# Optimization experiments

Measured on AMD Instinct MI355X. Metric: run time of the kernel, lower is better.

## Reference

```python
import jax, jax.numpy as jnp
import numpy as np

BS = 2048; N = 16; IN = 128; H = 128; M = 64; A = 32; IMSG = 64; NNH = 256; NA = 30; CB = 64

def _lin(x, w, b):
    return x @ w.T + b

def _bn(x, g, b):
    # BatchNorm1d in training mode: batch statistics, biased variance, eps=1e-5
    m = x.mean(0)
    v = x.var(0)
    return (x - m) / jnp.sqrt(v + 1e-5) * g + b

_lrelu = jax.nn.leaky_relu  # default negative_slope=0.01 matches torch LeakyReLU


def setup_inputs() -> dict:
    key = jax.random.key(0)
    ks = iter(jax.random.split(key, 32))
    def w(shape):
        return jax.random.normal(next(ks), shape, jnp.float32) / np.sqrt(shape[-1]).astype(np.float32)
    R = BS * N
    return {
        'inputs': jax.random.normal(next(ks), (R, IN), jnp.float32),
        'hidden_state': jax.random.normal(next(ks), (R, H), jnp.float32),
        'latent_state': jax.random.normal(next(ks), (R, CB), jnp.float32),
        'eps': jax.random.normal(next(ks), (R, M), jnp.float32),
        'fc1_w': w((H, IN)), 'fc1_b': jnp.zeros((H,), jnp.float32),
        'w_ih': w((3 * H, H)), 'w_hh': w((3 * H, H)),
        'b_ih': jnp.zeros((3 * H,), jnp.float32), 'b_hh': jnp.zeros((3 * H,), jnp.float32),
        'lse_w1': w((H, CB)), 'lse_b1': jnp.zeros((H,), jnp.float32),
        'lse_w2': w((H, H)), 'lse_b2': jnp.zeros((H,), jnp.float32),
        'me_w1': w((NNH, 2 * H)), 'me_b1': jnp.zeros((NNH,), jnp.float32),
        'me_g': jnp.ones((NNH,), jnp.float32), 'me_beta': jnp.zeros((NNH,), jnp.float32),
        'me_w2': w((2 * M, NNH)), 'me_b2': jnp.zeros((2 * M,), jnp.float32),
        'k_w': w((A, H)), 'k_b': jnp.zeros((A,), jnp.float32),
        'q_w': w((A, M)), 'q_b': jnp.zeros((A,), jnp.float32),
        'v_w1': w((NNH, H + M)), 'v_b1': jnp.zeros((NNH,), jnp.float32),
        'v_w2': w((IMSG, NNH)), 'v_b2': jnp.zeros((IMSG,), jnp.float32),
        'fc2_w': w((NA, 2 * H + IMSG * N)), 'fc2_b': jnp.zeros((NA,), jnp.float32),
        'n_agents': N,
    }


def reference(inputs, hidden_state, latent_state, eps,
              fc1_w, fc1_b, w_ih, w_hh, b_ih, b_hh,
              lse_w1, lse_b1, lse_w2, lse_b2,
              me_w1, me_b1, me_g, me_beta, me_w2, me_b2,
              k_w, k_b, q_w, q_b, v_w1, v_b1, v_w2, v_b2,
              fc2_w, fc2_b, n_agents):
    n = n_agents
    R = inputs.shape[0]
    bs = R // n
    # calc_hidden: fc1 + relu, then GRUCell
    x = jax.nn.relu(_lin(inputs, fc1_w, fc1_b))
    gi = _lin(x, w_ih, b_ih)
    gh = _lin(hidden_state, w_hh, b_hh)
    ir, iz, inn = jnp.split(gi, 3, axis=-1)
    hr, hz, hn = jnp.split(gh, 3, axis=-1)
    r = jax.nn.sigmoid(ir + hr)
    z = jax.nn.sigmoid(iz + hz)
    ng = jnp.tanh(inn + r * hn)
    h = ng + z * (hidden_state - ng)  # [R, H]
    # latent_state_encoder
    latent_emb = _lin(jax.nn.relu(_lin(latent_state, lse_w1, lse_b1)), lse_w2, lse_b2)
    le_d = jax.lax.stop_gradient(latent_emb)  # .detach() in source
    # msg_encoder -> clamped Normal params -> rsample
    t = _lrelu(_bn(_lin(jnp.concatenate([h, le_d], -1), me_w1, me_b1), me_g, me_beta))
    t = _lrelu(_lin(t, me_w2, me_b2))
    Md = eps.shape[-1]
    mean = jnp.clip(t[:, :Md], -1.0, 1.0)
    std = jnp.clip(t[:, Md:], 0.5, 1.0)
    pm = mean + std * eps  # personal_msg per agent, [R, M]
    # attn_message_integration: value/query at pair (i,j) depend only on sender j,
    # so compute once per sender and broadcast (same math as repeat in source).
    value = _lin(_lrelu(_lin(jnp.concatenate([h, pm], -1), v_w1, v_b1)), v_w2, v_b2).reshape(bs, n, -1)
    keyv = _lin(h, k_w, k_b).reshape(bs, n, -1)
    qv = _lin(pm, q_w, q_b).reshape(bs, n, -1)
    kh = keyv / jnp.maximum(jnp.linalg.norm(keyv, axis=-1, keepdims=True), 1e-8)
    qh = qv / jnp.maximum(jnp.linalg.norm(qv, axis=-1, keepdims=True), 1e-8)
    alpha = jax.nn.softmax(jnp.einsum('bia,bja->bij', kh, qh), axis=-1)  # cosine attn
    diag_mask = 1.0 - jnp.eye(n, dtype=alpha.dtype)  # zero self-messages
    msg = (alpha * diag_mask)[..., None] * value[:, None, :, :]  # [bs, n, n, IMSG]
    msg = msg.reshape(R, -1)
    return _lin(jnp.concatenate([h, latent_emb, msg], -1), fc2_w, fc2_b)  # q: [R, NA]
```

## Files before the change

kernel.cpp:

```cpp
#include <hip/hip_runtime.h>
#include <math.h>

namespace {
constexpr int R_ = 32768;
constexpr int N_ = 16;
constexpr int NA_ = 30;
constexpr int BSB_ = R_ / N_;
constexpr int NB64_ = R_ / 64;
}

typedef __bf16 bf16x8 __attribute__((ext_vector_type(8)));
typedef float f32x4 __attribute__((ext_vector_type(4)));

__device__ inline unsigned int f2bf(float f) {
    unsigned int u = __float_as_uint(f);
    return (u + 0x7fffu + ((u >> 16) & 1u)) >> 16;
}
__device__ inline float bf2f(unsigned int us) {
    return __uint_as_float(us << 16);
}
__device__ inline unsigned int pack2(float a, float b) {
    return f2bf(a) | (f2bf(b) << 16);
}
__device__ inline uint4 pack8(float4 f0, float4 f1) {
    uint4 u;
    u.x = pack2(f0.x, f0.y); u.y = pack2(f0.z, f0.w);
    u.z = pack2(f1.x, f1.y); u.w = pack2(f1.z, f1.w);
    return u;
}
__device__ inline float fsig(float x)  { return __builtin_amdgcn_rcpf(1.f + __expf(-x)); }
__device__ inline float ftanh(float x) { return 1.f - 2.f * __builtin_amdgcn_rcpf(__expf(2.f * x) + 1.f); }

__device__ __forceinline__ bf16x8 lda_frag(const uint4* At, int KC, int row, int c) {
    return __builtin_bit_cast(bf16x8, At[(row * KC + c) ^ (row & 7)]);
}
__device__ __forceinline__ bf16x8 ldb_frag(const unsigned short* W, int row, int rstride, int c) {
    return __builtin_bit_cast(bf16x8, *(const uint4*)(W + (size_t)row * rstride + (size_t)c * 8));
}

namespace woff {
constexpr unsigned fc1 = 0;
constexpr unsigned ih  = 16384;
constexpr unsigned hh  = 65536;
constexpr unsigned l1  = 114688;
constexpr unsigned l2  = 122880;
constexpr unsigned m1  = 139264;
constexpr unsigned m2  = 204800;
constexpr unsigned kw  = 237568;
constexpr unsigned qw  = 241664;
constexpr unsigned v1  = 243712;
constexpr unsigned v2  = 292864;
constexpr unsigned f2  = 309248;
constexpr unsigned total = 347648;
}

__global__ __launch_bounds__(256)
void wcvt_kernel(const float* __restrict__ fc1_w, const float* __restrict__ w_ih,
                 const float* __restrict__ w_hh, const float* __restrict__ lse_w1,
                 const float* __restrict__ lse_w2, const float* __restrict__ me_w1,
                 const float* __restrict__ me_w2, const float* __restrict__ k_w,
                 const float* __restrict__ q_w, const float* __restrict__ v_w1,
                 const float* __restrict__ v_w2, const float* __restrict__ fc2_w,
                 unsigned short* __restrict__ dst)
{
    unsigned i = blockIdx.x * 256 + threadIdx.x;
    if (i >= woff::total) return;
    const float* src; unsigned base;
    if      (i < woff::ih) { src = fc1_w;  base = woff::fc1; }
    else if (i < woff::hh) { src = w_ih;   base = woff::ih; }
    else if (i < woff::l1) { src = w_hh;   base = woff::hh; }
    else if (i < woff::l2) { src = lse_w1; base = woff::l1; }
    else if (i < woff::m1) { src = lse_w2; base = woff::l2; }
    else if (i < woff::m2) { src = me_w1;  base = woff::m1; }
    else if (i < woff::kw) { src = me_w2;  base = woff::m2; }
    else if (i < woff::qw) { src = k_w;    base = woff::kw; }
    else if (i < woff::v1) { src = q_w;    base = woff::qw; }
    else if (i < woff::v2) { src = v_w1;   base = woff::v1; }
    else if (i < woff::f2) { src = v_w2;   base = woff::v2; }
    else                   { src = fc2_w;  base = woff::f2; }
    dst[i] = (unsigned short)f2bf(src[i - base]);
}

__global__ __launch_bounds__(512, 4)
void stage1(const float* __restrict__ inputs, const float* __restrict__ hidden,
            const unsigned short* __restrict__ fc1w, const float* __restrict__ fc1_b,
            const unsigned short* __restrict__ wih, const unsigned short* __restrict__ whh,
            const float* __restrict__ b_ih, const float* __restrict__ b_hh,
            unsigned short* __restrict__ hb,
            const float* __restrict__ latent,
            const unsigned short* __restrict__ w1b, const float* __restrict__ b1,
            const unsigned short* __restrict__ w2b, const float* __restrict__ b2,
            unsigned short* __restrict__ leb)
{
    __shared__ uint4 shbuf[64 * 48];
    const int tid = threadIdx.x;
    const int lane = tid & 63, w = tid >> 6;
    const int m = lane & 15, g = lane >> 4;

    if (blockIdx.x < (unsigned)NB64_) {
        uint4* Ain   = shbuf;
        uint4* Atile = shbuf + 64 * 16;
        const int r0 = blockIdx.x * 64;

        for (int idx = tid; idx < 64 * 16; idx += 512) {
            int row = idx >> 4, c = idx & 15;
            const float4* p = (const float4*)(inputs + (size_t)(r0 + row) * 128 + c * 8);
            Ain[(row * 16 + c) ^ (row & 7)] = pack8(p[0], p[1]);
            const float4* ph = (const float4*)(hidden + (size_t)(r0 + row) * 128 + c * 8);
            Atile[(row * 32 + (16 + c)) ^ (row & 7)] = pack8(ph[0], ph[1]);
        }
        __syncthreads();

        {
            f32x4 acc[4] = {};
            #pragma unroll
            for (int ks = 0; ks < 4; ++ks) {
                bf16x8 bf = ldb_frag(fc1w, w * 16 + m, 128, ks * 4 + g);
                #pragma unroll
                for (int fr = 0; fr < 4; ++fr) {
                    bf16x8 af = lda_frag(Ain, 16, fr * 16 + m, ks * 4 + g);
                    acc[fr] = __builtin_amdgcn_mfma_f32_16x16x32_bf16(af, bf, acc[fr], 0, 0, 0);
                }
            }
            int col = w * 16 + m;
            float bv = fc1_b[col];
            int c = col >> 3, el = col & 7;
            #pragma unroll
            for (int fr = 0; fr < 4; ++fr) {
                #pragma unroll
                for (int i = 0; i < 4; ++i) {
                    int row = fr * 16 + g * 4 + i;
                    float v = acc[fr][i] + bv;
                    v = v > 0.f ? v : 0.f;
                    ((unsigned short*)Atile)[((row * 32 + c) ^ (row & 7)) * 8 + el] =
                        (unsigned short)f2bf(v);
                }
            }
        }
        __syncthreads();

        {
            f32x4 rr[4] = {}, zz[4] = {}, ni[4] = {}, nh[4] = {};
            const int ro = w * 16 + m;
            #pragma unroll
            for (int ks = 0; ks < 4; ++ks) {
                bf16x8 brr = ldb_frag(wih, ro, 128, ks * 4 + g);
                bf16x8 bzz = ldb_frag(wih, 128 + ro, 128, ks * 4 + g);
                bf16x8 bnn = ldb_frag(wih, 256 + ro, 128, ks * 4 + g);
                #pragma unroll
                for (int fr = 0; fr < 4; ++fr) {
                    bf16x8 af = lda_frag(Atile, 32, fr * 16 + m, ks * 4 + g);
                    rr[fr] = __builtin_amdgcn_mfma_f32_16x16x32_bf16(af, brr, rr[fr], 0, 0, 0);
                    zz[fr] = __builtin_amdgcn_mfma_f32_16x16x32_bf16(af, bzz, zz[fr], 0, 0, 0);
                    ni[fr] = __builtin_amdgcn_mfma_f32_16x16x32_bf16(af, bnn, ni[fr], 0, 0, 0);
                }
            }
            #pragma unroll
            for (int ks = 0; ks < 4; ++ks) {
                bf16x8 brr = ldb_frag(whh, ro, 128, ks * 4 + g);
                bf16x8 bzz = ldb_frag(whh, 128 + ro, 128, ks * 4 + g);
                bf16x8 bnn = ldb_frag(whh, 256 + ro, 128, ks * 4 + g);
                #pragma unroll
                for (int fr = 0; fr < 4; ++fr) {
                    bf16x8 af = lda_frag(Atile, 32, fr * 16 + m, 16 + ks * 4 + g);
                    rr[fr] = __builtin_amdgcn_mfma_f32_16x16x32_bf16(af, brr, rr[fr], 0, 0, 0);
                    zz[fr] = __builtin_amdgcn_mfma_f32_16x16x32_bf16(af, bzz, zz[fr], 0, 0, 0);
                    nh[fr] = __builtin_amdgcn_mfma_f32_16x16x32_bf16(af, bnn, nh[fr], 0, 0, 0);
                }
            }
            {
                int c = ro;
                float brz = b_ih[c] + b_hh[c];
                float bzz2 = b_ih[128 + c] + b_hh[128 + c];
                float bin = b_ih[256 + c], bhn = b_hh[256 + c];
                int hc = 16 + (c >> 3), hel = c & 7;
                #pragma unroll
                for (int fr = 0; fr < 4; ++fr) {
                    #pragma unroll
                    for (int i = 0; i < 4; ++i) {
                        int row = fr * 16 + g * 4 + i;
                        float rv = fsig(rr[fr][i] + brz);
                        float zv = fsig(zz[fr][i] + bzz2);
                        float ng = ftanh(ni[fr][i] + bin + rv * (nh[fr][i] + bhn));
                        float hp = bf2f(((unsigned short*)Atile)[((row * 32 + hc) ^ (row & 7)) * 8 + hel]);
                        float hv = ng + zv * (hp - ng);
                        hb[(size_t)(r0 + row) * 128 + c] = (unsigned short)f2bf(hv);
                    }
                }
            }
        }
    } else {
        uint4* Alat = shbuf;
        uint4* Alt  = shbuf + 64 * 8;
        const int r0 = (blockIdx.x - NB64_) * 64;

        {
            int row = tid >> 3, c = tid & 7;
            const float4* p = (const float4*)(latent + (size_t)(r0 + row) * 64 + c * 8);
            Alat[(row * 8 + c) ^ (row & 7)] = pack8(p[0], p[1]);
        }
        __syncthreads();

        {
            f32x4 acc[4] = {};
            #pragma unroll
            for (int ks = 0; ks < 2; ++ks) {
                bf16x8 bf = ldb_frag(w1b, w * 16 + m, 64, ks * 4 + g);
                #pragma unroll
                for (int fr = 0; fr < 4; ++fr) {
                    bf16x8 af = lda_frag(Alat, 8, fr * 16 + m, ks * 4 + g);
                    acc[fr] = __builtin_amdgcn_mfma_f32_16x16x32_bf16(af, bf, acc[fr], 0, 0, 0);
                }
            }
            int col = w * 16 + m;
            float bv = b1[col];
            int c = col >> 3, el = col & 7;
            #pragma unroll
            for (int fr = 0; fr < 4; ++fr) {
                #pragma unroll
                for (int i = 0; i < 4; ++i) {
                    int row = fr * 16 + g * 4 + i;
                    float v = acc[fr][i] + bv;
                    v = v > 0.f ? v : 0.f;
                    ((unsigned short*)Alt)[((row * 16 + c) ^ (row & 7)) * 8 + el] =
                        (unsigned short)f2bf(v);
                }
            }
        }
        __syncthreads();

        {
            f32x4 acc[4] = {};
            #pragma unroll
            for (int ks = 0; ks < 4; ++ks) {
                bf16x8 bf = ldb_frag(w2b, w * 16 + m, 128, ks * 4 + g);
                #pragma unroll
                for (int fr = 0; fr < 4; ++fr) {
                    bf16x8 af = lda_frag(Alt, 16, fr * 16 + m, ks * 4 + g);
                    acc[fr] = __builtin_amdgcn_mfma_f32_16x16x32_bf16(af, bf, acc[fr], 0, 0, 0);
                }
            }
            int col = w * 16 + m;
            float bv = b2[col];
            #pragma unroll
            for (int fr = 0; fr < 4; ++fr) {
                #pragma unroll
                for (int i = 0; i < 4; ++i) {
                    int rowl = fr * 16 + g * 4 + i;
                    float v = acc[fr][i] + bv;
                    leb[(size_t)(r0 + rowl) * 128 + col] = (unsigned short)f2bf(v);
                }
            }
        }
    }
}

__global__ __launch_bounds__(512, 4)
void me1_stats(const unsigned short* __restrict__ hb, const unsigned short* __restrict__ leb,
               const unsigned short* __restrict__ W, const float* __restrict__ bias,
               const unsigned short* __restrict__ f2w, const float* __restrict__ fc2_b,
               unsigned short* __restrict__ t1,
               float* __restrict__ psum, float* __restrict__ psq,
               float* __restrict__ hl)
{
    __shared__ uint4 Atile[64 * 32];
    __shared__ uint4 T1b[64 * 32];
    const int tid = threadIdx.x;
    const int r0 = blockIdx.x * 64;

    for (int idx = tid; idx < 64 * 16; idx += 512) {
        int row = idx >> 4, c = idx & 15;
        Atile[(row * 32 + c) ^ (row & 7)] =
            *(const uint4*)(hb + (size_t)(r0 + row) * 128 + c * 8);
        Atile[(row * 32 + (16 + c)) ^ (row & 7)] =
            *(const uint4*)(leb + (size_t)(r0 + row) * 128 + c * 8);
    }
    __syncthreads();

    const int lane = tid & 63, w = tid >> 6;
    const int m = lane & 15, g = lane >> 4;
    unsigned short* t1s = (unsigned short*)T1b;

    {
        const int o0 = w * 32;
        f32x4 acc[4][2] = {};
        #pragma unroll
        for (int ks = 0; ks < 8; ++ks) {
            bf16x8 bf[2];
            #pragma unroll
            for (int fc = 0; fc < 2; ++fc)
                bf[fc] = ldb_frag(W, o0 + fc * 16 + m, 256, ks * 4 + g);
            #pragma unroll
            for (int fr = 0; fr < 4; ++fr) {
                bf16x8 af = lda_frag(Atile, 32, fr * 16 + m, ks * 4 + g);
                #pragma unroll
                for (int fc = 0; fc < 2; ++fc)
                    acc[fr][fc] = __builtin_amdgcn_mfma_f32_16x16x32_bf16(
                        af, bf[fc], acc[fr][fc], 0, 0, 0);
            }
        }
        #pragma unroll
        for (int fc = 0; fc < 2; ++fc) {
            int col = o0 + fc * 16 + m;
            float bv = bias[col];
            float s = 0.f, q = 0.f;
            #pragma unroll
            for (int fr = 0; fr < 4; ++fr) {
                #pragma unroll
                for (int i = 0; i < 4; ++i) {
                    int rowl = fr * 16 + g * 4 + i;
                    float v = acc[fr][fc][i] + bv;
                    t1s[rowl * 256 + col] = (unsigned short)f2bf(v);
                    s += v; q += v * v;
                }
            }
            s += __shfl_xor(s, 16); s += __shfl_xor(s, 32);
            q += __shfl_xor(q, 16); q += __shfl_xor(q, 32);
            if (lane < 16) {
                psum[(size_t)blockIdx.x * 256 + col] = s;
                psq[(size_t)blockIdx.x * 256 + col] = q;
            }
        }
    }
    __syncthreads();
    for (int idx = tid; idx < 64 * 32; idx += 512) {
        int row = idx >> 5, c = idx & 31;
        *(uint4*)(t1 + (size_t)(r0 + row) * 256 + c * 8) = T1b[row * 32 + c];
    }

    if (w < 4) {
        f32x4 acc[2] = {};
        #pragma unroll
        for (int ks = 0; ks < 8; ++ks) {
            bf16x8 af = lda_frag(Atile, 32, w * 16 + m, ks * 4 + g);
            bf16x8 bf[2];
            #pragma unroll
            for (int fc = 0; fc < 2; ++fc) {
                int col = fc * 16 + m;
                bf[fc] = (col < NA_) ? ldb_frag(f2w, col, 1280, ks * 4 + g) : bf16x8{};
            }
            #pragma unroll
            for (int fc = 0; fc < 2; ++fc)
                acc[fc] = __builtin_amdgcn_mfma_f32_16x16x32_bf16(af, bf[fc], acc[fc], 0, 0, 0);
        }
        #pragma unroll
        for (int fc = 0; fc < 2; ++fc) {
            int col = fc * 16 + m;
            if (col < NA_) {
                float bv = fc2_b[col];
                #pragma unroll
                for (int i = 0; i < 4; ++i) {
                    int row = r0 + w * 16 + g * 4 + i;
                    hl[(size_t)row * NA_ + col] = acc[fc][i] + bv;
                }
            }
        }
    }
}

__global__ __launch_bounds__(256)
void bn_final_kernel(const float* __restrict__ psum, const float* __restrict__ psq,
                     const float* __restrict__ g, const float* __restrict__ beta,
                     float* __restrict__ scale, float* __restrict__ shift)
{
    __shared__ float redS[4], redQ[4];
    const int f = blockIdx.x;
    const int tid = threadIdx.x;
    float s = 0.f, q = 0.f;
    for (int b = tid; b < NB64_; b += 256) {
        s += psum[(size_t)b * 256 + f];
        q += psq[(size_t)b * 256 + f];
    }
    #pragma unroll
    for (int off = 32; off >= 1; off >>= 1) {
        s += __shfl_down(s, off);
        q += __shfl_down(q, off);
    }
    if ((tid & 63) == 0) { redS[tid >> 6] = s; redQ[tid >> 6] = q; }
    __syncthreads();
    if (tid == 0) {
        s = redS[0] + redS[1] + redS[2] + redS[3];
        q = redQ[0] + redQ[1] + redQ[2] + redQ[3];
        float mean = s / (float)R_;
        float var = q / (float)R_ - mean * mean;
        float istd = rsqrtf(var + 1e-5f);
        float sc = g[f] * istd;
        scale[f] = sc;
        shift[f] = beta[f] - mean * sc;
    }
}

__global__ __launch_bounds__(512, 4)
void me2kqv(const unsigned short* __restrict__ t1,
            const float* __restrict__ scale, const float* __restrict__ shift,
            const unsigned short* __restrict__ W2, const float* __restrict__ me2_b,
            const float* __restrict__ eps,
            const unsigned short* __restrict__ hb,
            const unsigned short* __restrict__ kwb, const float* __restrict__ k_b,
            const unsigned short* __restrict__ qwb, const float* __restrict__ q_b,
            const unsigned short* __restrict__ v1w, const float* __restrict__ v1_b,
            const unsigned short* __restrict__ v2w, const float* __restrict__ v2_b,
            float* __restrict__ kh, float* __restrict__ qh,
            unsigned short* __restrict__ valb)
{
    __shared__ uint4 bufA[64 * 32];
    __shared__ uint4 bufB[64 * 24];
    __shared__ float sc_s[256], sh_s[256];
    const int tid = threadIdx.x;
    const int r0 = blockIdx.x * 64;
    const int lane = tid & 63, w = tid >> 6;
    const int m = lane & 15, g = lane >> 4;

    if (tid < 256) { sc_s[tid] = scale[tid]; sh_s[tid] = shift[tid]; }
    for (int idx = tid; idx < 64 * 16; idx += 512) {
        int row = idx >> 4, c = idx & 15;
        bufB[(row * 24 + c) ^ (row & 7)] =
            *(const uint4*)(hb + (size_t)(r0 + row) * 128 + c * 8);
    }
    __syncthreads();

    for (int idx = tid; idx < 64 * 32; idx += 512) {
        int row = idx >> 5, c = idx & 31;
        uint4 u = *(const uint4*)(t1 + (size_t)(r0 + row) * 256 + c * 8);
        unsigned int vv[4] = {u.x, u.y, u.z, u.w};
        float f[8];
        #pragma unroll
        for (int q2 = 0; q2 < 4; ++q2) {
            f[2 * q2]     = __uint_as_float((vv[q2] & 0xffffu) << 16);
            f[2 * q2 + 1] = __uint_as_float(vv[q2] & 0xffff0000u);
        }
        int k = c * 8;
        #pragma unroll
        for (int j = 0; j < 8; ++j) {
            float v = f[j] * sc_s[k + j] + sh_s[k + j];
            f[j] = v > 0.f ? v : 0.01f * v;
        }
        uint4 r;
        r.x = pack2(f[0], f[1]); r.y = pack2(f[2], f[3]);
        r.z = pack2(f[4], f[5]); r.w = pack2(f[6], f[7]);
        bufA[(row * 32 + c) ^ (row & 7)] = r;
    }
    __syncthreads();

    {
        const int colm = w * 16 + m;
        f32x4 acc[4] = {};
        #pragma unroll
        for (int ks = 0; ks < 8; ++ks) {
            bf16x8 bf = ldb_frag(W2, colm, 256, ks * 4 + g);
            #pragma unroll
            for (int fr = 0; fr < 4; ++fr) {
                bf16x8 af = lda_frag(bufA, 32, fr * 16 + m, ks * 4 + g);
                acc[fr] = __builtin_amdgcn_mfma_f32_16x16x32_bf16(af, bf, acc[fr], 0, 0, 0);
            }
        }
        float bv = me2_b[colm];
        __syncthreads();
        float* meanS = (float*)bufA;
        if (w < 4) {
            #pragma unroll
            for (int fr = 0; fr < 4; ++fr) {
                #pragma unroll
                for (int i = 0; i < 4; ++i) {
                    int row = fr * 16 + g * 4 + i;
                    float vm = acc[fr][i] + bv;
                    vm = vm > 0.f ? vm : 0.01f * vm;
                    vm = fminf(fmaxf(vm, -1.f), 1.f);
                    meanS[row * 64 + colm] = vm;
                }
            }
        }
        __syncthreads();
        if (w >= 4) {
            int cp = colm - 64;
            int hc = 16 + (cp >> 3), hel = cp & 7;
            #pragma unroll
            for (int fr = 0; fr < 4; ++fr) {
                #pragma unroll
                for (int i = 0; i < 4; ++i) {
                    int row = fr * 16 + g * 4 + i;
                    float vs = acc[fr][i] + bv;
                    vs = vs > 0.f ? vs : 0.01f * vs;
                    vs = fminf(fmaxf(vs, 0.5f), 1.f);
                    float e = eps[(size_t)(r0 + row) * 64 + cp];
                    float vm = meanS[row * 64 + cp];
                    ((unsigned short*)bufB)[((row * 24 + hc) ^ (row & 7)) * 8 + hel] =
                        (unsigned short)f2bf(vm + vs * e);
                }
            }
        }
    }
    __syncthreads();

    if (w < 4) {
        const bool isq = (w >= 2);
        const int rbase = (w & 1) * 32;
        f32x4 acc[2][2] = {};
        const int nks = isq ? 2 : 4;
        for (int ks = 0; ks < nks; ++ks) {
            bf16x8 af[2], bf[2];
            #pragma unroll
            for (int fr = 0; fr < 2; ++fr)
                af[fr] = lda_frag(bufB, 24, rbase + fr * 16 + m, (isq ? 16 : 0) + ks * 4 + g);
            #pragma unroll
            for (int fc = 0; fc < 2; ++fc)
                bf[fc] = isq ? ldb_frag(qwb, fc * 16 + m, 64, ks * 4 + g)
                             : ldb_frag(kwb, fc * 16 + m, 128, ks * 4 + g);
            #pragma unroll
            for (int fr = 0; fr < 2; ++fr)
                #pragma unroll
                for (int fc = 0; fc < 2; ++fc)
                    acc[fr][fc] = __builtin_amdgcn_mfma_f32_16x16x32_bf16(
                        af[fr], bf[fc], acc[fr][fc], 0, 0, 0);
        }
        const float* bias = isq ? q_b : k_b;
        float b0 = bias[m], b1 = bias[16 + m];
        float* outp = isq ? qh : kh;
        #pragma unroll
        for (int fr = 0; fr < 2; ++fr) {
            #pragma unroll
            for (int i = 0; i < 4; ++i) {
                float v0 = acc[fr][0][i] + b0;
                float v1 = acc[fr][1][i] + b1;
                float ss = v0 * v0 + v1 * v1;
                ss += __shfl_xor(ss, 1); ss += __shfl_xor(ss, 2);
                ss += __shfl_xor(ss, 4); ss += __shfl_xor(ss, 8);
                float inv = 1.f / fmaxf(sqrtf(ss), 1e-8f);
                int row = r0 + rbase + fr * 16 + g * 4 + i;
                outp[(size_t)row * 32 + m] = v0 * inv;
                outp[(size_t)row * 32 + 16 + m] = v1 * inv;
            }
        }
    }

    {
        const int o0 = w * 32;
        f32x4 acc[4][2] = {};
        #pragma unroll
        for (int ks = 0; ks < 6; ++ks) {
            bf16x8 bf[2];
            #pragma unroll
            for (int fc = 0; fc < 2; ++fc)
                bf[fc] = ldb_frag(v1w, o0 + fc * 16 + m, 192, ks * 4 + g);
            #pragma unroll
            for (int fr = 0; fr < 4; ++fr) {
                bf16x8 af = lda_frag(bufB, 24, fr * 16 + m, ks * 4 + g);
                #pragma unroll
                for (int fc = 0; fc < 2; ++fc)
                    acc[fr][fc] = __builtin_amdgcn_mfma_f32_16x16x32_bf16(
                        af, bf[fc], acc[fr][fc], 0, 0, 0);
            }
        }
        #pragma unroll
        for (int fc = 0; fc < 2; ++fc) {
            int col = o0 + fc * 16 + m;
            float bv = v1_b[col];
            int c = col >> 3, el = col & 7;
            #pragma unroll
            for (int fr = 0; fr < 4; ++fr) {
                #pragma unroll
                for (int i = 0; i < 4; ++i) {
                    int row = fr * 16 + g * 4 + i;
                    float v = acc[fr][fc][i] + bv;
                    v = v > 0.f ? v : 0.01f * v;
                    ((unsigned short*)bufA)[((row * 32 + c) ^ (row & 7)) * 8 + el] =
                        (unsigned short)f2bf(v);
                }
            }
        }
    }
    __syncthreads();

    {
        const int col = (w & 3) * 16 + m;
        const int rbase = (w >> 2) * 32;
        f32x4 acc[2] = {};
        #pragma unroll
        for (int ks = 0; ks < 8; ++ks) {
            bf16x8 bf = ldb_frag(v2w, col, 256, ks * 4 + g);
            #pragma unroll
            for (int fr = 0; fr < 2; ++fr) {
                bf16x8 af = lda_frag(bufA, 32, rbase + fr * 16 + m, ks * 4 + g);
                acc[fr] = __builtin_amdgcn_mfma_f32_16x16x32_bf16(af, bf, acc[fr], 0, 0, 0);
            }
        }
        float bv = v2_b[col];
        unsigned short* vb = (unsigned short*)bufB;
        #pragma unroll
        for (int fr = 0; fr < 2; ++fr) {
            #pragma unroll
            for (int i = 0; i < 4; ++i) {
                int rowl = rbase + fr * 16 + g * 4 + i;
                vb[rowl * 64 + col] = (unsigned short)f2bf(acc[fr][i] + bv);
            }
        }
    }
    __syncthreads();
    {
        int row = tid >> 3, c = tid & 7;
        *(uint4*)(valb + (size_t)(r0 + row) * 64 + c * 8) = ((uint4*)bufB)[row * 8 + c];
    }
}

__global__ __launch_bounds__(256)
void vproj_kernel(const unsigned short* __restrict__ value, const float* __restrict__ w2,
                  float* __restrict__ vproj)
{
    __shared__ float w2s[NA_][65];
    __shared__ float val_s[64][65];
    const int tid = threadIdx.x;
    const int j = blockIdx.x & 15;
    const int b0 = (blockIdx.x >> 4) * 64;

    for (int idx = tid; idx < NA_ * 64; idx += 256) {
        int na = idx >> 6, k = idx & 63;
        w2s[na][k] = w2[(size_t)na * 1280 + 256 + j * 64 + k];
    }
    for (int idx = tid; idx < 64 * 64; idx += 256) {
        int bl = idx >> 6, k = idx & 63;
        val_s[bl][k] = bf2f(value[((size_t)(b0 + bl) * 16 + j) * 64 + k]);
    }
    __syncthreads();

    for (int task = tid; task < 64 * NA_; task += 256) {
        int bl = task / NA_, na = task - bl * NA_;
        float acc = 0.f;
        #pragma unroll 16
        for (int k = 0; k < 64; ++k) acc = fmaf(val_s[bl][k], w2s[na][k], acc);
        vproj[((size_t)(b0 + bl) * 16 + j) * NA_ + na] = acc;
    }
}

__global__ __launch_bounds__(256)
void attn_combine(const float* __restrict__ kh, const float* __restrict__ qh,
                  const float* __restrict__ vproj, const float* __restrict__ hl,
                  float* __restrict__ outv)
{
    __shared__ float kh_s[16][33], qh_s[16][33];
    __shared__ float al_s[16][16];
    __shared__ float vp_s[16][NA_];
    const int tid = threadIdx.x;
    const size_t rb = (size_t)blockIdx.x * 16;

    for (int idx = tid; idx < 512; idx += 256) {
        int r = idx >> 5, a = idx & 31;
        kh_s[r][a] = kh[rb * 32 + idx];
        qh_s[r][a] = qh[rb * 32 + idx];
    }
    for (int idx = tid; idx < 16 * NA_; idx += 256)
        vp_s[idx / NA_][idx % NA_] = vproj[rb * NA_ + idx];
    __syncthreads();

    {
        int i = tid >> 4, j = tid & 15;
        float l = 0.f;
        #pragma unroll
        for (int a = 0; a < 32; ++a) l = fmaf(kh_s[i][a], qh_s[j][a], l);
        float mx = l;
        #pragma unroll
        for (int mm = 8; mm >= 1; mm >>= 1) mx = fmaxf(mx, __shfl_xor(mx, mm));
        float e = __expf(l - mx);
        float s = e;
        #pragma unroll
        for (int mm = 8; mm >= 1; mm >>= 1) s += __shfl_xor(s, mm);
        float a = e / s;
        if (i == j) a = 0.f;
        al_s[i][j] = a;
    }
    __syncthreads();

    for (int task = tid; task < 16 * NA_; task += 256) {
        int i = task / NA_, na = task - i * NA_;
        float acc = hl[(rb + i) * NA_ + na];
        #pragma unroll
        for (int j = 0; j < 16; ++j) acc = fmaf(al_s[i][j], vp_s[j][na], acc);
        outv[(rb + i) * NA_ + na] = acc;
    }
}

extern "C" void kernel_launch(void* const* d_in, const int* in_sizes, int n_in,
                              void* d_out, int out_size, void* d_ws, size_t ws_size,
                              hipStream_t stream)
{
    (void)in_sizes; (void)n_in; (void)out_size; (void)ws_size;
    const float* inputs  = (const float*)d_in[0];
    const float* hidden  = (const float*)d_in[1];
    const float* latent  = (const float*)d_in[2];
    const float* eps     = (const float*)d_in[3];
    const float* fc1_w   = (const float*)d_in[4];
    const float* fc1_b   = (const float*)d_in[5];
    const float* w_ih    = (const float*)d_in[6];
    const float* w_hh    = (const float*)d_in[7];
    const float* b_ih    = (const float*)d_in[8];
    const float* b_hh    = (const float*)d_in[9];
    const float* lse_w1  = (const float*)d_in[10];
    const float* lse_b1  = (const float*)d_in[11];
    const float* lse_w2  = (const float*)d_in[12];
    const float* lse_b2  = (const float*)d_in[13];
    const float* me_w1   = (const float*)d_in[14];
    const float* me_b1   = (const float*)d_in[15];
    const float* me_g    = (const float*)d_in[16];
    const float* me_beta = (const float*)d_in[17];
    const float* me_w2   = (const float*)d_in[18];
    const float* me_b2   = (const float*)d_in[19];
    const float* k_w     = (const float*)d_in[20];
    const float* k_b     = (const float*)d_in[21];
    const float* q_w     = (const float*)d_in[22];
    const float* q_b     = (const float*)d_in[23];
    const float* v_w1    = (const float*)d_in[24];
    const float* v_b1    = (const float*)d_in[25];
    const float* v_w2    = (const float*)d_in[26];
    const float* v_b2    = (const float*)d_in[27];
    const float* fc2_w   = (const float*)d_in[28];
    const float* fc2_b   = (const float*)d_in[29];

    const size_t R = R_;
    unsigned short* bws = (unsigned short*)d_ws;
    unsigned short* hb   = bws;
    unsigned short* leb  = hb + R * 128;
    unsigned short* t1b  = leb + R * 128;
    unsigned short* valb = t1b + R * 256;
    unsigned short* wb   = valb + R * 64;
    float* fws  = (float*)(wb + woff::total);
    float* khf  = fws;
    float* qhf  = khf + R * 32;
    float* hlf  = qhf + R * 32;
    float* vpf  = hlf + R * 30;
    float* psum = vpf + R * 30;
    float* psq  = psum + (size_t)NB64_ * 256;
    float* scale = psq + (size_t)NB64_ * 256;
    float* shift = scale + 256;

    dim3 blk(256);
    dim3 g512(NB64_);

    wcvt_kernel<<<dim3((woff::total + 255) / 256), blk, 0, stream>>>(
        fc1_w, w_ih, w_hh, lse_w1, lse_w2, me_w1, me_w2, k_w, q_w, v_w1, v_w2, fc2_w, wb);

    stage1<<<dim3(2 * NB64_), dim3(512), 0, stream>>>(
        inputs, hidden, wb + woff::fc1, fc1_b, wb + woff::ih, wb + woff::hh,
        b_ih, b_hh, hb,
        latent, wb + woff::l1, lse_b1, wb + woff::l2, lse_b2, leb);
    me1_stats<<<g512, dim3(512), 0, stream>>>(hb, leb, wb + woff::m1, me_b1,
                                              wb + woff::f2, fc2_b, t1b, psum, psq, hlf);
    bn_final_kernel<<<dim3(256), blk, 0, stream>>>(psum, psq, me_g, me_beta, scale, shift);
    me2kqv<<<g512, dim3(512), 0, stream>>>(t1b, scale, shift, wb + woff::m2, me_b2, eps,
                                           hb, wb + woff::kw, k_b, wb + woff::qw, q_b,
                                           wb + woff::v1, v_b1, wb + woff::v2, v_b2,
                                           khf, qhf, valb);
    vproj_kernel<<<dim3(16 * (BSB_ / 64)), blk, 0, stream>>>(valb, fc2_w, vpf);
    attn_combine<<<dim3(BSB_), blk, 0, stream>>>(khf, qhf, vpf, hlf, (float*)d_out);
}
```

Before: 110.0 us.

## Fuse value projection and attention combine into me2 kernel tail

Folds vproj_kernel and attn_combine into the end of the me2kqv kernel, now called me2tail. Each 64-row block holds four complete 16-agent groups, so kh/qh stay in shared memory and the value-times-fc2 projection and softmax attention run locally. This removes two launches and the global round-trips of kh, qh, value and vproj. In exchange it adds shared memory (khs/qhs arrays), which may lower occupancy. The vproj step now reads fc2 weights as fp32 straight from global per thread instead of staging them in shared memory.

```diff
diff --git a/kernel.cpp b/kernel.cpp
--- a/kernel.cpp
+++ b/kernel.cpp
@@ -391,20 +391,21 @@
 }
 
 __global__ __launch_bounds__(512, 4)
-void me2kqv(const unsigned short* __restrict__ t1,
-            const float* __restrict__ scale, const float* __restrict__ shift,
-            const unsigned short* __restrict__ W2, const float* __restrict__ me2_b,
-            const float* __restrict__ eps,
-            const unsigned short* __restrict__ hb,
-            const unsigned short* __restrict__ kwb, const float* __restrict__ k_b,
-            const unsigned short* __restrict__ qwb, const float* __restrict__ q_b,
-            const unsigned short* __restrict__ v1w, const float* __restrict__ v1_b,
-            const unsigned short* __restrict__ v2w, const float* __restrict__ v2_b,
-            float* __restrict__ kh, float* __restrict__ qh,
-            unsigned short* __restrict__ valb)
+void me2tail(const unsigned short* __restrict__ t1,
+             const float* __restrict__ scale, const float* __restrict__ shift,
+             const unsigned short* __restrict__ W2, const float* __restrict__ me2_b,
+             const float* __restrict__ eps,
+             const unsigned short* __restrict__ hb,
+             const unsigned short* __restrict__ kwb, const float* __restrict__ k_b,
+             const unsigned short* __restrict__ qwb, const float* __restrict__ q_b,
+             const unsigned short* __restrict__ v1w, const float* __restrict__ v1_b,
+             const unsigned short* __restrict__ v2w, const float* __restrict__ v2_b,
+             const float* __restrict__ w2f, const float* __restrict__ hl,
+             float* __restrict__ outv)
 {
     __shared__ uint4 bufA[64 * 32];
     __shared__ uint4 bufB[64 * 24];
+    __shared__ float khs[64][33], qhs[64][33];
     __shared__ float sc_s[256], sh_s[256];
     const int tid = threadIdx.x;
     const int r0 = blockIdx.x * 64;
@@ -515,7 +516,6 @@
         }
         const float* bias = isq ? q_b : k_b;
         float b0 = bias[m], b1 = bias[16 + m];
-        float* outp = isq ? qh : kh;
         #pragma unroll
         for (int fr = 0; fr < 2; ++fr) {
             #pragma unroll
@@ -526,9 +526,9 @@
                 ss += __shfl_xor(ss, 1); ss += __shfl_xor(ss, 2);
                 ss += __shfl_xor(ss, 4); ss += __shfl_xor(ss, 8);
                 float inv = 1.f / fmaxf(sqrtf(ss), 1e-8f);
-                int row = r0 + rbase + fr * 16 + g * 4 + i;
-                outp[(size_t)row * 32 + m] = v0 * inv;
-                outp[(size_t)row * 32 + 16 + m] = v1 * inv;
+                int row = rbase + fr * 16 + g * 4 + i;
+                if (isq) { qhs[row][m] = v0 * inv; qhs[row][16 + m] = v1 * inv; }
+                else     { khs[row][m] = v0 * inv; khs[row][16 + m] = v1 * inv; }
             }
         }
     }
@@ -596,85 +596,59 @@
         }
     }
     __syncthreads();
+
+    float* vp = (float*)bufA;
+    float* al = vp + 64 * 32;
     {
-        int row = tid >> 3, c = tid & 7;
-        *(uint4*)(valb + (size_t)(r0 + row) * 64 + c * 8) = ((uint4*)bufB)[row * 8 + c];
-    }
-}
-
-__global__ __launch_bounds__(256)
-void vproj_kernel(const unsigned short* __restrict__ value, const float* __restrict__ w2,
-                  float* __restrict__ vproj)
-{
-    __shared__ float w2s[NA_][65];
-    __shared__ float val_s[64][65];
-    const int tid = threadIdx.x;
-    const int j = blockIdx.x & 15;
-    const int b0 = (blockIdx.x >> 4) * 64;
-
-    for (int idx = tid; idx < NA_ * 64; idx += 256) {
-        int na = idx >> 6, k = idx & 63;
-        w2s[na][k] = w2[(size_t)na * 1280 + 256 + j * 64 + k];
-    }
-    for (int idx = tid; idx < 64 * 64; idx += 256) {
-        int bl = idx >> 6, k = idx & 63;
-        val_s[bl][k] = bf2f(value[((size_t)(b0 + bl) * 16 + j) * 64 + k]);
-    }
-    __syncthreads();
-
-    for (int task = tid; task < 64 * NA_; task += 256) {
-        int bl = task / NA_, na = task - bl * NA_;
-        float acc = 0.f;
-        #pragma unroll 16
-        for (int k = 0; k < 64; ++k) acc = fmaf(val_s[bl][k], w2s[na][k], acc);
-        vproj[((size_t)(b0 + bl) * 16 + j) * NA_ + na] = acc;
-    }
-}
-
-__global__ __launch_bounds__(256)
-void attn_combine(const float* __restrict__ kh, const float* __restrict__ qh,
-                  const float* __restrict__ vproj, const float* __restrict__ hl,
-                  float* __restrict__ outv)
-{
-    __shared__ float kh_s[16][33], qh_s[16][33];
-    __shared__ float al_s[16][16];
-    __shared__ float vp_s[16][NA_];
-    const int tid = threadIdx.x;
-    const size_t rb = (size_t)blockIdx.x * 16;
-
-    for (int idx = tid; idx < 512; idx += 256) {
-        int r = idx >> 5, a = idx & 31;
-        kh_s[r][a] = kh[rb * 32 + idx];
-        qh_s[r][a] = qh[rb * 32 + idx];
-    }
-    for (int idx = tid; idx < 16 * NA_; idx += 256)
-        vp_s[idx / NA_][idx % NA_] = vproj[rb * NA_ + idx];
-    __syncthreads();
-
-    {
-        int i = tid >> 4, j = tid & 15;
-        float l = 0.f;
-        #pragma unroll
-        for (int a = 0; a < 32; ++a) l = fmaf(kh_s[i][a], qh_s[j][a], l);
-        float mx = l;
-        #pragma unroll
-        for (int mm = 8; mm >= 1; mm >>= 1) mx = fmaxf(mx, __shfl_xor(mx, mm));
-        float e = __expf(l - mx);
-        float s = e;
-        #pragma unroll
-        for (int mm = 8; mm >= 1; mm >>= 1) s += __shfl_xor(s, mm);
-        float a = e / s;
-        if (i == j) a = 0.f;
-        al_s[i][j] = a;
-    }
-    __syncthreads();
-
-    for (int task = tid; task < 16 * NA_; task += 256) {
-        int i = task / NA_, na = task - i * NA_;
-        float acc = hl[(rb + i) * NA_ + na];
-        #pragma unroll
-        for (int j = 0; j < 16; ++j) acc = fmaf(al_s[i][j], vp_s[j][na], acc);
-        outv[(rb + i) * NA_ + na] = acc;
+        const unsigned short* vb = (const unsigned short*)bufB;
+        for (int task = tid; task < 64 * NA_; task += 512) {
+            int row = task / NA_, na = task - row * NA_;
+            int j = row & 15;
+            const float* wp = w2f + (size_t)na * 1280 + 256 + j * 64;
+            float acc = 0.f;
+            #pragma unroll
+            for (int k8 = 0; k8 < 8; ++k8) {
+                uint4 uv = *(const uint4*)(vb + row * 64 + k8 * 8);
+                float4 w0 = *(const float4*)(wp + k8 * 8);
+                float4 w1 = *(const float4*)(wp + k8 * 8 + 4);
+                acc += bf2f(uv.x & 0xffffu) * w0.x + bf2f(uv.x >> 16) * w0.y;
+                acc += bf2f(uv.y & 0xffffu) * w0.z + bf2f(uv.y >> 16) * w0.w;
+                acc += bf2f(uv.z & 0xffffu) * w1.x + bf2f(uv.z >> 16) * w1.y;
+                acc += bf2f(uv.w & 0xffffu) * w1.z + bf2f(uv.w >> 16) * w1.w;
+            }
+            vp[row * 32 + na] = acc;
+        }
+        #pragma unroll
+        for (int base = 0; base < 1024; base += 512) {
+            int idx = base + tid;
+            int rowi = idx >> 4;
+            int j = idx & 15;
+            int qrow = (rowi & 48) | j;
+            float l = 0.f;
+            #pragma unroll
+            for (int a = 0; a < 32; ++a) l = fmaf(khs[rowi][a], qhs[qrow][a], l);
+            float mx = l;
+            #pragma unroll
+            for (int mm = 8; mm >= 1; mm >>= 1) mx = fmaxf(mx, __shfl_xor(mx, mm));
+            float e = __expf(l - mx);
+            float s = e;
+            #pragma unroll
+            for (int mm = 8; mm >= 1; mm >>= 1) s += __shfl_xor(s, mm);
+            float a = e / s;
+            if ((rowi & 15) == j) a = 0.f;
+            al[rowi * 16 + j] = a;
+        }
+    }
+    __syncthreads();
+
+    for (int task = tid; task < 64 * NA_; task += 512) {
+        int rowi = task / NA_, na = task - rowi * NA_;
+        int b16 = rowi & 48;
+        float acc = hl[(size_t)(r0 + rowi) * NA_ + na];
+        #pragma unroll
+        for (int j = 0; j < 16; ++j)
+            acc = fmaf(al[rowi * 16 + j], vp[(b16 + j) * 32 + na], acc);
+        outv[(size_t)(r0 + rowi) * NA_ + na] = acc;
     }
 }
 
@@ -719,14 +693,10 @@
     unsigned short* hb   = bws;
     unsigned short* leb  = hb + R * 128;
     unsigned short* t1b  = leb + R * 128;
-    unsigned short* valb = t1b + R * 256;
-    unsigned short* wb   = valb + R * 64;
+    unsigned short* wb   = t1b + R * 256;
     float* fws  = (float*)(wb + woff::total);
-    float* khf  = fws;
-    float* qhf  = khf + R * 32;
-    float* hlf  = qhf + R * 32;
-    float* vpf  = hlf + R * 30;
-    float* psum = vpf + R * 30;
+    float* hlf  = fws;
+    float* psum = hlf + R * 30;
     float* psq  = psum + (size_t)NB64_ * 256;
     float* scale = psq + (size_t)NB64_ * 256;
     float* shift = scale + 256;
@@ -744,10 +714,8 @@
     me1_stats<<<g512, dim3(512), 0, stream>>>(hb, leb, wb + woff::m1, me_b1,
                                               wb + woff::f2, fc2_b, t1b, psum, psq, hlf);
     bn_final_kernel<<<dim3(256), blk, 0, stream>>>(psum, psq, me_g, me_beta, scale, shift);
-    me2kqv<<<g512, dim3(512), 0, stream>>>(t1b, scale, shift, wb + woff::m2, me_b2, eps,
-                                           hb, wb + woff::kw, k_b, wb + woff::qw, q_b,
-                                           wb + woff::v1, v_b1, wb + woff::v2, v_b2,
-                                           khf, qhf, valb);
-    vproj_kernel<<<dim3(16 * (BSB_ / 64)), blk, 0, stream>>>(valb, fc2_w, vpf);
-    attn_combine<<<dim3(BSB_), blk, 0, stream>>>(khf, qhf, vpf, hlf, (float*)d_out);
-}
+    me2tail<<<g512, dim3(512), 0, stream>>>(t1b, scale, shift, wb + woff::m2, me_b2, eps,
+                                            hb, wb + woff::kw, k_b, wb + woff::qw, q_b,
+                                            wb + woff::v1, v_b1, wb + woff::v2, v_b2,
+                                            fc2_w, hlf, (float*)d_out);
+}
```

Measured after the change: 119.6 us. 1.09x slower.
